# Kernel tuning notes

Measured on AMD Instinct MI355X. Metric: run time of the kernel, lower is better.

The kernel has to match this reference:

```python
import jax, jax.numpy as jnp
import numpy as np

EMBED_DIM = 1024
NUM_HEADS = 16
HEAD_DIM = EMBED_DIM // NUM_HEADS
B, N = 4, 2048


def setup_inputs() -> dict:
    key = jax.random.key(0)
    ks = jax.random.split(key, 12)
    s = 1.0 / np.sqrt(EMBED_DIM)
    inp = {
        "x": jax.random.normal(ks[0], (B, N, EMBED_DIM), dtype=jnp.float32),
        "dist_matrix": jax.random.uniform(ks[1], (N, N), dtype=jnp.float32),
        # Linear weights stored torch-style [out, in]
        "Wq": jax.random.normal(ks[2], (EMBED_DIM, EMBED_DIM), dtype=jnp.float32) * s,
        "bq": jnp.zeros((EMBED_DIM,), dtype=jnp.float32),
        "Wk": jax.random.normal(ks[3], (EMBED_DIM, EMBED_DIM), dtype=jnp.float32) * s,
        "bk": jnp.zeros((EMBED_DIM,), dtype=jnp.float32),
        "Wv": jax.random.normal(ks[4], (EMBED_DIM, EMBED_DIM), dtype=jnp.float32) * s,
        "bv": jnp.zeros((EMBED_DIM,), dtype=jnp.float32),
        "Wo": jax.random.normal(ks[5], (EMBED_DIM, EMBED_DIM), dtype=jnp.float32) * s,
        "bo": jnp.zeros((EMBED_DIM,), dtype=jnp.float32),
        # DistanceBias params: bias = dist_w * dist + dist_b (learned scalar affine)
        "dist_w": jnp.asarray(-1.0, dtype=jnp.float32),
        "dist_b": jnp.asarray(0.0, dtype=jnp.float32),
    }
    return inp


def reference(x, dist_matrix, Wq, bq, Wk, bk, Wv, bv, Wo, bo, dist_w, dist_b):
    b, n, c = x.shape
    h, d = NUM_HEADS, HEAD_DIM
    # projections (torch Linear: x @ W.T + b), reshape to [b, h, n, d]
    def proj(W, bias):
        y = jnp.einsum('bnc,oc->bno', x, W) + bias
        return y.reshape(b, n, h, d).transpose(0, 2, 1, 3)
    q = proj(Wq, bq)
    k = proj(Wk, bk)
    v = proj(Wv, bv)
    scores = jnp.einsum('bhnd,bhmd->bhnm', q, k) / np.sqrt(d).astype(np.float32)
    bias = dist_w * dist_matrix + dist_b            # [N, N], shared over b, h
    scores = scores + bias[None, None, :, :]
    attn = jax.nn.softmax(scores, axis=-1)
    out = jnp.einsum('bhnm,bhmd->bhnd', attn, v)    # [b, h, n, d]
    out = out.transpose(0, 2, 1, 3).reshape(b, n, c)
    return jnp.einsum('bnc,oc->bno', out, Wo) + bo
```

## Files before the change

kernel.cpp:

```cpp
#include <hip/hip_runtime.h>
#include <stdint.h>

typedef unsigned short ushort;
typedef __attribute__((ext_vector_type(8))) short bf16x8;
typedef __attribute__((ext_vector_type(4))) float f32x4;
typedef __attribute__((ext_vector_type(16))) float f32x16;

__device__ __forceinline__ float b2f(ushort u) {
    return __uint_as_float(((unsigned)u) << 16);
}
__device__ __forceinline__ ushort f2b(float f) {
    unsigned u = __float_as_uint(f);
    u += 0x7fff + ((u >> 16) & 1);
    return (ushort)(u >> 16);
}

#if __has_builtin(__builtin_amdgcn_exp2f)
#define EXP2(x) __builtin_amdgcn_exp2f(x)
#else
#define EXP2(x) __expf((x) * 0.69314718056f)
#endif

__device__ __forceinline__ unsigned cvtpk(float a, float b) {
    unsigned r;
    asm("v_cvt_pk_bf16_f32 %0, %1, %2" : "=v"(r) : "v"(a), "v"(b));
    return r;
}

__device__ __forceinline__ void plswap(unsigned &a, unsigned &b) {
#if __has_builtin(__builtin_amdgcn_permlane32_swap)
    auto r = __builtin_amdgcn_permlane32_swap(a, b, 0, 0);
    a = (unsigned)r[0]; b = (unsigned)r[1];
#else
    asm volatile("v_permlane32_swap_b32 %0, %1" : "+v"(a), "+v"(b));
#endif
}

#define SEQN 2048
#define EMB  1024
#define NH   16
#define HD   64
#define BHSTRIDE (SEQN * HD)

__device__ __forceinline__ void gload16(const ushort* g, ushort* l) {
    __builtin_amdgcn_global_load_lds(
        (const __attribute__((address_space(1))) unsigned int*)g,
        (__attribute__((address_space(3))) unsigned int*)l, 16, 0, 0);
}

__global__ __launch_bounds__(256) void conv_x(
        const float* __restrict__ s, ushort* __restrict__ d) {
    const size_t i = (size_t)blockIdx.x * 256 + threadIdx.x;
    float4 a = ((const float4*)s)[2 * i];
    float4 b = ((const float4*)s)[2 * i + 1];
    ushort pk[8] = {f2b(a.x), f2b(a.y), f2b(a.z), f2b(a.w),
                    f2b(b.x), f2b(b.y), f2b(b.z), f2b(b.w)};
    ((uint4*)d)[i] = *(uint4*)pk;
}

__global__ __launch_bounds__(256) void conv_w4(
        const float* __restrict__ W0, const float* __restrict__ W1,
        const float* __restrict__ W2, const float* __restrict__ W3,
        ushort* __restrict__ d) {
    const float* s = (blockIdx.y == 0) ? W0 : (blockIdx.y == 1) ? W1
                   : (blockIdx.y == 2) ? W2 : W3;
    ushort* dst = d + ((size_t)blockIdx.y << 20);
    const size_t i = (size_t)blockIdx.x * 256 + threadIdx.x;
    float4 a = ((const float4*)s)[2 * i];
    float4 b = ((const float4*)s)[2 * i + 1];
    ushort pk[8] = {f2b(a.x), f2b(a.y), f2b(a.z), f2b(a.w),
                    f2b(b.x), f2b(b.y), f2b(b.z), f2b(b.w)};
    ((uint4*)dst)[i] = *(uint4*)pk;
}

__global__ __launch_bounds__(256) void conv_Lp(
        const float* __restrict__ dist, const float* __restrict__ dw,
        const float* __restrict__ db, float* __restrict__ Lp) {
    const float c1 = dw[0] * 1.44269504f, c2 = db[0] * 1.44269504f;
    const size_t gid = (size_t)blockIdx.x * 256 + threadIdx.x;
    const int lo  = (int)(gid & 31);
    const int kv4 = (int)((gid >> 5) & 511);
    const int qt  = (int)(gid >> 14);
    const int q   = qt * 32 + lo;
    float4 d = *(const float4*)(dist + (size_t)q * SEQN + kv4 * 4);
    float4 o = {fmaf(d.x, c1, c2), fmaf(d.y, c1, c2),
                fmaf(d.z, c1, c2), fmaf(d.w, c1, c2)};
    ((float4*)Lp)[gid] = o;
}

#define LDSZ (128 * 32)

__global__ __launch_bounds__(256) void gemm_qkv(
        const ushort* __restrict__ xb, const ushort* __restrict__ Wb,
        const float* __restrict__ bq, const float* __restrict__ bk,
        const float* __restrict__ bv,
        ushort* __restrict__ qb, ushort* __restrict__ kb,
        ushort* __restrict__ vT) {
    __shared__ ushort As[LDSZ];
    __shared__ ushort Bs[LDSZ];
    const int m0   = blockIdx.x * 128;
    const int nt   = blockIdx.y;
    const int wsel = nt >> 3;
    const int n0   = (nt & 7) * 128;
    const ushort* W    = Wb + ((size_t)wsel << 20);
    const float* bias  = (wsel == 0) ? bq : (wsel == 1) ? bk : bv;

    const int t = threadIdx.x, lane = t & 63, wave = t >> 6;
    const int ln = lane & 15, quad = lane >> 4;
    const int wm = wave & 1, wn = wave >> 1;

    const int e0 = wave * 128 + lane;
    const int e1 = e0 + 64;
    const ushort* gA0 = xb + (size_t)(m0 + (e0 >> 2)) * 1024 + (e0 & 3) * 8;
    const ushort* gA1 = xb + (size_t)(m0 + (e1 >> 2)) * 1024 + (e1 & 3) * 8;
    const ushort* gB0 = W  + (size_t)(n0 + (e0 >> 2)) * 1024 + (e0 & 3) * 8;
    const ushort* gB1 = W  + (size_t)(n0 + (e1 >> 2)) * 1024 + (e1 & 3) * 8;
    ushort* lA0 = As + wave * 1024;
    ushort* lA1 = lA0 + 512;
    ushort* lB0 = Bs + wave * 1024;
    ushort* lB1 = lB0 + 512;

    f32x4 acc[4][4];
#pragma unroll
    for (int i = 0; i < 4; i++)
#pragma unroll
        for (int j = 0; j < 4; j++) acc[i][j] = (f32x4){0.f, 0.f, 0.f, 0.f};

    for (int k0 = 0; k0 < 1024; k0 += 32) {
        __syncthreads();
        gload16(gA0 + k0, lA0);
        gload16(gA1 + k0, lA1);
        gload16(gB0 + k0, lB0);
        gload16(gB1 + k0, lB1);
        __syncthreads();
        bf16x8 af[4], bfr[4];
#pragma unroll
        for (int i = 0; i < 4; i++)
            af[i]  = *(bf16x8*)&As[(wm * 64 + i * 16 + ln) * 32 + quad * 8];
#pragma unroll
        for (int j = 0; j < 4; j++)
            bfr[j] = *(bf16x8*)&Bs[(wn * 64 + j * 16 + ln) * 32 + quad * 8];
#pragma unroll
        for (int i = 0; i < 4; i++)
#pragma unroll
            for (int j = 0; j < 4; j++)
                acc[i][j] = __builtin_amdgcn_mfma_f32_16x16x32_bf16(
                                af[i], bfr[j], acc[i][j], 0, 0, 0);
    }

    if (wsel < 2) {
        ushort* dst = (wsel == 0) ? qb : kb;
        const float scale = (wsel == 0) ? 0.125f : 1.0f;
#pragma unroll
        for (int j = 0; j < 4; j++) {
            const int o  = n0 + wn * 64 + j * 16 + ln;
            const float bval = bias[o];
            const int h = o >> 6, d = o & 63;
#pragma unroll
            for (int i = 0; i < 4; i++) {
                const int mg = m0 + wm * 64 + i * 16 + quad * 4;
#pragma unroll
                for (int r = 0; r < 4; r++) {
                    const int m  = mg + r;
                    const int b  = m >> 11;
                    const int ns = m & 2047;
                    dst[(size_t)(b * NH + h) * BHSTRIDE + (size_t)ns * HD + d] =
                        f2b((acc[i][j][r] + bval) * scale);
                }
            }
        }
    } else {
#pragma unroll
        for (int j = 0; j < 4; j++) {
            const int o  = n0 + wn * 64 + j * 16 + ln;
            const float bval = bias[o];
            const int h = o >> 6, d = o & 63;
#pragma unroll
            for (int i = 0; i < 4; i++) {
                const int mg = m0 + wm * 64 + i * 16 + quad * 4;
                const int b  = mg >> 11;
                const int ns = mg & 2047;
                ushort pk[4];
#pragma unroll
                for (int r = 0; r < 4; r++) pk[r] = f2b(acc[i][j][r] + bval);
                *(uint2*)&vT[(size_t)(b * NH + h) * BHSTRIDE +
                             (size_t)d * SEQN + ns] = *(uint2*)&pk[0];
            }
        }
    }
}

__global__ __launch_bounds__(256, 4) void attn(
        ushort* q,
        const ushort* __restrict__ k,
        const ushort* __restrict__ vT,
        const float* __restrict__ Lp) {
    __shared__ short Ks[2][64 * 72];
    __shared__ short Vs[2][64 * 72];
    const int t = threadIdx.x, lane = t & 63, wave = t >> 6;
    const int lo = lane & 31, hi = lane >> 5;
    const int h = blockIdx.y, b = blockIdx.z;
    const int bh = b * NH + h;
    const int qw0 = blockIdx.x * 128 + wave * 32;

    ushort* qp = q + (size_t)bh * BHSTRIDE;
    const ushort* kp = k  + (size_t)bh * BHSTRIDE;
    const ushort* vp = vT + (size_t)bh * BHSTRIDE;
    const float4* Lp4 = (const float4*)Lp + ((size_t)(qw0 >> 5) * 512) * 32 + lo;

    const int sr = t >> 2;
    const int sc = (t & 3) * 16;

    bf16x8 qf[4];
#pragma unroll
    for (int kk = 0; kk < 4; kk++)
        qf[kk] = *(const bf16x8*)(qp + (size_t)(qw0 + lo) * HD + kk * 16 + hi * 8);

    f32x16 O[2];
#pragma unroll
    for (int dt = 0; dt < 2; dt++)
#pragma unroll
        for (int i = 0; i < 16; i++) O[dt][i] = 0.f;
    float lsum = 0.f;

    uint4 krg0 = *(const uint4*)(kp + (size_t)sr * HD + sc);
    uint4 krg1 = *(const uint4*)(kp + (size_t)sr * HD + sc + 8);
    uint4 vrg0 = *(const uint4*)(vp + (size_t)sr * SEQN + sc);
    uint4 vrg1 = *(const uint4*)(vp + (size_t)sr * SEQN + sc + 8);
    *(uint4*)&Ks[0][sr * 72 + sc]     = krg0;
    *(uint4*)&Ks[0][sr * 72 + sc + 8] = krg1;
    *(uint4*)&Vs[0][sr * 72 + sc]     = vrg0;
    *(uint4*)&Vs[0][sr * 72 + sc + 8] = vrg1;
    krg0 = *(const uint4*)(kp + (size_t)(64 + sr) * HD + sc);
    krg1 = *(const uint4*)(kp + (size_t)(64 + sr) * HD + sc + 8);
    vrg0 = *(const uint4*)(vp + (size_t)sr * SEQN + 64 + sc);
    vrg1 = *(const uint4*)(vp + (size_t)sr * SEQN + 64 + sc + 8);

    for (int kt = 0; kt < 32; kt++) {
        const int kv0 = kt * 64;
        const int cb = kt & 1;
        __syncthreads();
        *(uint4*)&Ks[cb ^ 1][sr * 72 + sc]     = krg0;
        *(uint4*)&Ks[cb ^ 1][sr * 72 + sc + 8] = krg1;
        *(uint4*)&Vs[cb ^ 1][sr * 72 + sc]     = vrg0;
        *(uint4*)&Vs[cb ^ 1][sr * 72 + sc + 8] = vrg1;
        const int kvn = (kv0 + 128) & 2047;
        krg0 = *(const uint4*)(kp + (size_t)(kvn + sr) * HD + sc);
        krg1 = *(const uint4*)(kp + (size_t)(kvn + sr) * HD + sc + 8);
        vrg0 = *(const uint4*)(vp + (size_t)sr * SEQN + kvn + sc);
        vrg1 = *(const uint4*)(vp + (size_t)sr * SEQN + kvn + sc + 8);
        float4 lv2[2][4];
#pragma unroll
        for (int s = 0; s < 2; s++)
#pragma unroll
            for (int n = 0; n < 4; n++)
                lv2[s][n] = Lp4[((kv0 >> 2) + s * 8 + hi + 2 * n) * 32];

#pragma unroll
        for (int s = 0; s < 2; s++) {
            f32x16 z;
#pragma unroll
            for (int i = 0; i < 16; i++) z[i] = 0.f;
            __builtin_amdgcn_s_setprio(1);
#pragma unroll
            for (int kk = 0; kk < 4; kk++) {
                bf16x8 kf = *(bf16x8*)&Ks[cb][(s * 32 + lo) * 72 + kk * 16 + hi * 8];
                z = __builtin_amdgcn_mfma_f32_32x32x16_bf16(kf, qf[kk], z, 0, 0, 0);
            }
            __builtin_amdgcn_s_setprio(0);
            float p[16];
#pragma unroll
            for (int n = 0; n < 4; n++) {
#pragma unroll
                for (int m = 0; m < 4; m++) {
                    float pv = EXP2(fmaf(z[n * 4 + m], 1.44269504f,
                                         ((const float*)&lv2[s][n])[m]));
                    lsum += pv;
                    p[n * 4 + m] = pv;
                }
            }
#pragma unroll
            for (int kl = 0; kl < 2; kl++) {
                unsigned a0 = cvtpk(p[kl * 8 + 0], p[kl * 8 + 1]);
                unsigned b0 = cvtpk(p[kl * 8 + 4], p[kl * 8 + 5]);
                plswap(a0, b0);
                unsigned a1 = cvtpk(p[kl * 8 + 2], p[kl * 8 + 3]);
                unsigned b1 = cvtpk(p[kl * 8 + 6], p[kl * 8 + 7]);
                plswap(a1, b1);
                union { bf16x8 v; unsigned u[4]; } pf;
                pf.u[0] = a0; pf.u[1] = a1; pf.u[2] = b0; pf.u[3] = b1;
                const int kvk = s * 2 + kl;
                __builtin_amdgcn_s_setprio(1);
#pragma unroll
                for (int dt = 0; dt < 2; dt++) {
                    bf16x8 vf = *(bf16x8*)&Vs[cb][(dt * 32 + lo) * 72 +
                                                  kvk * 16 + hi * 8];
                    O[dt] = __builtin_amdgcn_mfma_f32_32x32x16_bf16(
                                vf, pf.v, O[dt], 0, 0, 0);
                }
                __builtin_amdgcn_s_setprio(0);
            }
        }
    }

    float tot = lsum + __shfl_xor(lsum, 32);
    const float inv = 1.0f / tot;
#pragma unroll
    for (int dt = 0; dt < 2; dt++)
#pragma unroll
        for (int n = 0; n < 4; n++) {
            uint2 pk2;
            pk2.x = cvtpk(O[dt][n * 4 + 0] * inv, O[dt][n * 4 + 1] * inv);
            pk2.y = cvtpk(O[dt][n * 4 + 2] * inv, O[dt][n * 4 + 3] * inv);
            *(uint2*)(qp + (size_t)(qw0 + lo) * HD + dt * 32 + hi * 4 + n * 8)
                = pk2;
        }
}

__global__ __launch_bounds__(256) void gemm_out(
        const ushort* __restrict__ ao, const ushort* __restrict__ Wob,
        const float* __restrict__ bias, float* __restrict__ out) {
    __shared__ ushort As[LDSZ];
    __shared__ ushort Bs[LDSZ];
    const int m0 = blockIdx.x * 128;
    const int n0 = blockIdx.y * 128;
    const int t = threadIdx.x, lane = t & 63, wave = t >> 6;
    const int ln = lane & 15, quad = lane >> 4;
    const int wm = wave & 1, wn = wave >> 1;

    const int e0 = wave * 128 + lane;
    const int e1 = e0 + 64;
    const int bb = m0 >> 11;
    const int nbase = m0 & 2047;
    const ushort* gA0 = ao + ((size_t)bb << 21) +
                        (size_t)(nbase + (e0 >> 2)) * 64 + (e0 & 3) * 8;
    const ushort* gA1 = ao + ((size_t)bb << 21) +
                        (size_t)(nbase + (e1 >> 2)) * 64 + (e1 & 3) * 8;
    const ushort* gB0 = Wob + (size_t)(n0 + (e0 >> 2)) * 1024 + (e0 & 3) * 8;
    const ushort* gB1 = Wob + (size_t)(n0 + (e1 >> 2)) * 1024 + (e1 & 3) * 8;
    ushort* lA0 = As + wave * 1024;
    ushort* lA1 = lA0 + 512;
    ushort* lB0 = Bs + wave * 1024;
    ushort* lB1 = lB0 + 512;

    f32x4 acc[4][4];
#pragma unroll
    for (int i = 0; i < 4; i++)
#pragma unroll
        for (int j = 0; j < 4; j++) acc[i][j] = (f32x4){0.f, 0.f, 0.f, 0.f};

    for (int k0 = 0; k0 < 1024; k0 += 32) {
        const size_t aoff = ((size_t)(k0 >> 6) << 17) + (k0 & 32);
        __syncthreads();
        gload16(gA0 + aoff, lA0);
        gload16(gA1 + aoff, lA1);
        gload16(gB0 + k0, lB0);
        gload16(gB1 + k0, lB1);
        __syncthreads();
        bf16x8 af[4], bfr[4];
#pragma unroll
        for (int i = 0; i < 4; i++)
            af[i]  = *(bf16x8*)&As[(wm * 64 + i * 16 + ln) * 32 + quad * 8];
#pragma unroll
        for (int j = 0; j < 4; j++)
            bfr[j] = *(bf16x8*)&Bs[(wn * 64 + j * 16 + ln) * 32 + quad * 8];
#pragma unroll
        for (int i = 0; i < 4; i++)
#pragma unroll
            for (int j = 0; j < 4; j++)
                acc[i][j] = __builtin_amdgcn_mfma_f32_16x16x32_bf16(
                                af[i], bfr[j], acc[i][j], 0, 0, 0);
    }

#pragma unroll
    for (int j = 0; j < 4; j++) {
        const int o = n0 + wn * 64 + j * 16 + ln;
        const float bval = bias[o];
#pragma unroll
        for (int i = 0; i < 4; i++) {
            const int mg = m0 + wm * 64 + i * 16 + quad * 4;
#pragma unroll
            for (int r = 0; r < 4; r++)
                out[(size_t)(mg + r) * EMB + o] = acc[i][j][r] + bval;
        }
    }
}

extern "C" void kernel_launch(void* const* d_in, const int* in_sizes, int n_in,
                              void* d_out, int out_size, void* d_ws, size_t ws_size,
                              hipStream_t stream) {
    const float* x    = (const float*)d_in[0];
    const float* dist = (const float*)d_in[1];
    const float* Wq   = (const float*)d_in[2];
    const float* bq   = (const float*)d_in[3];
    const float* Wk   = (const float*)d_in[4];
    const float* bk   = (const float*)d_in[5];
    const float* Wv   = (const float*)d_in[6];
    const float* bv   = (const float*)d_in[7];
    const float* Wo   = (const float*)d_in[8];
    const float* bo   = (const float*)d_in[9];
    const float* dw   = (const float*)d_in[10];
    const float* db   = (const float*)d_in[11];

    const size_t PLANE = (size_t)8192 * 1024;
    ushort* qb = (ushort*)d_ws;
    ushort* kb = qb + PLANE;
    ushort* xb = kb + PLANE;
    ushort* Wb = xb + PLANE;
    ushort* vT = (ushort*)d_out;
    float*  Lf = (float*)(vT + PLANE);

    dim3 blk(256);
    conv_x       <<<dim3(4096),      blk, 0, stream>>>(x, xb);
    conv_w4      <<<dim3(512, 4),    blk, 0, stream>>>(Wq, Wk, Wv, Wo, Wb);
    conv_Lp      <<<dim3(4096),      blk, 0, stream>>>(dist, dw, db, Lf);
    gemm_qkv     <<<dim3(64, 24),    blk, 0, stream>>>(xb, Wb, bq, bk, bv,
                                                       qb, kb, vT);
    attn         <<<dim3(16, 16, 4), blk, 0, stream>>>(qb, kb, vT, Lf);
    gemm_out     <<<dim3(64, 8),     blk, 0, stream>>>(qb, Wb + 3 * (size_t)(1 << 20),
                                                       bo, (float*)d_out);
}
```

Baseline: 322.5 us.

## Double K-step per barrier in GEMMs and remap attention blocks across XCDs

Both projection GEMMs now load two 32-wide K slices per iteration into two LDS buffers, which halves the number of barrier pairs and doubles the loads in flight per sync. The attention kernel remaps its flat block id so that all query tiles of one batch-head land on the same XCD, improving L2 reuse of the K/V and bias data. The cost is twice the LDS use in the GEMMs and a remap that hard-codes the grid shape (16 query tiles, 64 heads, 8 XCDs).

```diff
diff --git a/kernel.cpp b/kernel.cpp
--- a/kernel.cpp
+++ b/kernel.cpp
@@ -96,8 +96,8 @@
         const float* __restrict__ bv,
         ushort* __restrict__ qb, ushort* __restrict__ kb,
         ushort* __restrict__ vT) {
-    __shared__ ushort As[LDSZ];
-    __shared__ ushort Bs[LDSZ];
+    __shared__ ushort As[2][LDSZ];
+    __shared__ ushort Bs[2][LDSZ];
     const int m0   = blockIdx.x * 128;
     const int nt   = blockIdx.y;
     const int wsel = nt >> 3;
@@ -115,10 +115,10 @@
     const ushort* gA1 = xb + (size_t)(m0 + (e1 >> 2)) * 1024 + (e1 & 3) * 8;
     const ushort* gB0 = W  + (size_t)(n0 + (e0 >> 2)) * 1024 + (e0 & 3) * 8;
     const ushort* gB1 = W  + (size_t)(n0 + (e1 >> 2)) * 1024 + (e1 & 3) * 8;
-    ushort* lA0 = As + wave * 1024;
-    ushort* lA1 = lA0 + 512;
-    ushort* lB0 = Bs + wave * 1024;
-    ushort* lB1 = lB0 + 512;
+    ushort* lA0a = &As[0][wave * 1024]; ushort* lA0b = lA0a + 512;
+    ushort* lA1a = &As[1][wave * 1024]; ushort* lA1b = lA1a + 512;
+    ushort* lB0a = &Bs[0][wave * 1024]; ushort* lB0b = lB0a + 512;
+    ushort* lB1a = &Bs[1][wave * 1024]; ushort* lB1b = lB1a + 512;
 
     f32x4 acc[4][4];
 #pragma unroll
@@ -126,26 +126,29 @@
 #pragma unroll
         for (int j = 0; j < 4; j++) acc[i][j] = (f32x4){0.f, 0.f, 0.f, 0.f};
 
-    for (int k0 = 0; k0 < 1024; k0 += 32) {
+    for (int k0 = 0; k0 < 1024; k0 += 64) {
         __syncthreads();
-        gload16(gA0 + k0, lA0);
-        gload16(gA1 + k0, lA1);
-        gload16(gB0 + k0, lB0);
-        gload16(gB1 + k0, lB1);
+        gload16(gA0 + k0,      lA0a); gload16(gA1 + k0,      lA0b);
+        gload16(gB0 + k0,      lB0a); gload16(gB1 + k0,      lB0b);
+        gload16(gA0 + k0 + 32, lA1a); gload16(gA1 + k0 + 32, lA1b);
+        gload16(gB0 + k0 + 32, lB1a); gload16(gB1 + k0 + 32, lB1b);
         __syncthreads();
-        bf16x8 af[4], bfr[4];
-#pragma unroll
-        for (int i = 0; i < 4; i++)
-            af[i]  = *(bf16x8*)&As[(wm * 64 + i * 16 + ln) * 32 + quad * 8];
-#pragma unroll
-        for (int j = 0; j < 4; j++)
-            bfr[j] = *(bf16x8*)&Bs[(wn * 64 + j * 16 + ln) * 32 + quad * 8];
-#pragma unroll
-        for (int i = 0; i < 4; i++)
+#pragma unroll
+        for (int kk2 = 0; kk2 < 2; kk2++) {
+            bf16x8 af[4], bfr[4];
+#pragma unroll
+            for (int i = 0; i < 4; i++)
+                af[i]  = *(bf16x8*)&As[kk2][(wm * 64 + i * 16 + ln) * 32 + quad * 8];
 #pragma unroll
             for (int j = 0; j < 4; j++)
-                acc[i][j] = __builtin_amdgcn_mfma_f32_16x16x32_bf16(
-                                af[i], bfr[j], acc[i][j], 0, 0, 0);
+                bfr[j] = *(bf16x8*)&Bs[kk2][(wn * 64 + j * 16 + ln) * 32 + quad * 8];
+#pragma unroll
+            for (int i = 0; i < 4; i++)
+#pragma unroll
+                for (int j = 0; j < 4; j++)
+                    acc[i][j] = __builtin_amdgcn_mfma_f32_16x16x32_bf16(
+                                    af[i], bfr[j], acc[i][j], 0, 0, 0);
+        }
     }
 
     if (wsel < 2) {
@@ -199,9 +202,12 @@
     __shared__ short Vs[2][64 * 72];
     const int t = threadIdx.x, lane = t & 63, wave = t >> 6;
     const int lo = lane & 31, hi = lane >> 5;
-    const int h = blockIdx.y, b = blockIdx.z;
-    const int bh = b * NH + h;
-    const int qw0 = blockIdx.x * 128 + wave * 32;
+    const int wid  = blockIdx.x + (blockIdx.y << 4) + (blockIdx.z << 8);
+    const int xcd  = wid & 7;
+    const int slot = wid >> 3;
+    const int bh   = xcd * 8 + (slot >> 4);
+    const int qx   = slot & 15;
+    const int qw0 = qx * 128 + wave * 32;
 
     ushort* qp = q + (size_t)bh * BHSTRIDE;
     const ushort* kp = k  + (size_t)bh * BHSTRIDE;
@@ -320,8 +326,8 @@
 __global__ __launch_bounds__(256) void gemm_out(
         const ushort* __restrict__ ao, const ushort* __restrict__ Wob,
         const float* __restrict__ bias, float* __restrict__ out) {
-    __shared__ ushort As[LDSZ];
-    __shared__ ushort Bs[LDSZ];
+    __shared__ ushort As[2][LDSZ];
+    __shared__ ushort Bs[2][LDSZ];
     const int m0 = blockIdx.x * 128;
     const int n0 = blockIdx.y * 128;
     const int t = threadIdx.x, lane = t & 63, wave = t >> 6;
@@ -338,10 +344,10 @@
                         (size_t)(nbase + (e1 >> 2)) * 64 + (e1 & 3) * 8;
     const ushort* gB0 = Wob + (size_t)(n0 + (e0 >> 2)) * 1024 + (e0 & 3) * 8;
     const ushort* gB1 = Wob + (size_t)(n0 + (e1 >> 2)) * 1024 + (e1 & 3) * 8;
-    ushort* lA0 = As + wave * 1024;
-    ushort* lA1 = lA0 + 512;
-    ushort* lB0 = Bs + wave * 1024;
-    ushort* lB1 = lB0 + 512;
+    ushort* lA0a = &As[0][wave * 1024]; ushort* lA0b = lA0a + 512;
+    ushort* lA1a = &As[1][wave * 1024]; ushort* lA1b = lA1a + 512;
+    ushort* lB0a = &Bs[0][wave * 1024]; ushort* lB0b = lB0a + 512;
+    ushort* lB1a = &Bs[1][wave * 1024]; ushort* lB1b = lB1a + 512;
 
     f32x4 acc[4][4];
 #pragma unroll
@@ -349,27 +355,30 @@
 #pragma unroll
         for (int j = 0; j < 4; j++) acc[i][j] = (f32x4){0.f, 0.f, 0.f, 0.f};
 
-    for (int k0 = 0; k0 < 1024; k0 += 32) {
-        const size_t aoff = ((size_t)(k0 >> 6) << 17) + (k0 & 32);
+    for (int k0 = 0; k0 < 1024; k0 += 64) {
+        const size_t aoff = ((size_t)(k0 >> 6) << 17);
         __syncthreads();
-        gload16(gA0 + aoff, lA0);
-        gload16(gA1 + aoff, lA1);
-        gload16(gB0 + k0, lB0);
-        gload16(gB1 + k0, lB1);
+        gload16(gA0 + aoff,      lA0a); gload16(gA1 + aoff,      lA0b);
+        gload16(gB0 + k0,        lB0a); gload16(gB1 + k0,        lB0b);
+        gload16(gA0 + aoff + 32, lA1a); gload16(gA1 + aoff + 32, lA1b);
+        gload16(gB0 + k0 + 32,   lB1a); gload16(gB1 + k0 + 32,   lB1b);
         __syncthreads();
-        bf16x8 af[4], bfr[4];
-#pragma unroll
-        for (int i = 0; i < 4; i++)
-            af[i]  = *(bf16x8*)&As[(wm * 64 + i * 16 + ln) * 32 + quad * 8];
-#pragma unroll
-        for (int j = 0; j < 4; j++)
-            bfr[j] = *(bf16x8*)&Bs[(wn * 64 + j * 16 + ln) * 32 + quad * 8];
-#pragma unroll
-        for (int i = 0; i < 4; i++)
+#pragma unroll
+        for (int kk2 = 0; kk2 < 2; kk2++) {
+            bf16x8 af[4], bfr[4];
+#pragma unroll
+            for (int i = 0; i < 4; i++)
+                af[i]  = *(bf16x8*)&As[kk2][(wm * 64 + i * 16 + ln) * 32 + quad * 8];
 #pragma unroll
             for (int j = 0; j < 4; j++)
-                acc[i][j] = __builtin_amdgcn_mfma_f32_16x16x32_bf16(
-                                af[i], bfr[j], acc[i][j], 0, 0, 0);
+                bfr[j] = *(bf16x8*)&Bs[kk2][(wn * 64 + j * 16 + ln) * 32 + quad * 8];
+#pragma unroll
+            for (int i = 0; i < 4; i++)
+#pragma unroll
+                for (int j = 0; j < 4; j++)
+                    acc[i][j] = __builtin_amdgcn_mfma_f32_16x16x32_bf16(
+                                    af[i], bfr[j], acc[i][j], 0, 0, 0);
+        }
     }
 
 #pragma unroll
```

Result: faster. 315.3 us (-2.2%).
